# Performance work log

Hardware: AMD Instinct MI355X
Metric: run time of the kernel (lower is better)

The kernel has to match this reference:

```python
import jax, jax.numpy as jnp
import numpy as np

N_NODES = 90  # hard-coded per-graph node count in the original module
HIDDEN = 128


def setup_inputs() -> dict:
    key = jax.random.key(0)
    ks = jax.random.split(key, 12)
    B = 8192
    adj = jax.random.uniform(ks[0], (B, N_NODES, N_NODES), dtype=jnp.float32)
    s_in = 1.0 / np.sqrt(N_NODES)
    s_h = 1.0 / np.sqrt(HIDDEN)
    return {
        "adj": adj,
        "W_mlp0": jax.random.normal(ks[1], (N_NODES, HIDDEN), jnp.float32) * s_in,
        "b_mlp0": jax.random.normal(ks[2], (HIDDEN,), jnp.float32) * s_in,
        "W_mlp1": jax.random.normal(ks[3], (HIDDEN, HIDDEN), jnp.float32) * s_h,
        "b_mlp1": jax.random.normal(ks[4], (HIDDEN,), jnp.float32) * s_h,
        "W_mlp2": jax.random.normal(ks[5], (HIDDEN, HIDDEN), jnp.float32) * s_h,
        "b_mlp2": jax.random.normal(ks[6], (HIDDEN,), jnp.float32) * s_h,
        "W_res1": jax.random.normal(ks[7], (HIDDEN, HIDDEN), jnp.float32) * s_h,
        "b_res1": jax.random.normal(ks[8], (HIDDEN,), jnp.float32) * s_h,
        "W_res2": jax.random.normal(ks[9], (HIDDEN, HIDDEN), jnp.float32) * s_h,
        "b_res2": jax.random.normal(ks[10], (HIDDEN,), jnp.float32) * s_h,
    }


def reference(adj, W_mlp0, b_mlp0, W_mlp1, b_mlp1, W_mlp2, b_mlp2,
              W_res1, b_res1, W_res2, b_res2):
    B = adj.shape[0]
    # raw node features: identity per graph (torch.eye(90) concatenated)
    raw_x = jnp.broadcast_to(jnp.eye(N_NODES, dtype=adj.dtype), (B, N_NODES, N_NODES))

    def gconv(x, W, b):
        # block-diagonal Adj_block @ x == batched per-graph matmul, then linear
        return jnp.einsum('bij,bjk->bik', adj, x) @ W + b

    # encoding == 1 branch, layers = 3
    h0 = gconv(raw_x, W_mlp0, b_mlp0)                    # mlps[0](raw_x, A)
    r1 = h0 @ W_res1 + b_res1                            # res[1](h0)
    x = jax.nn.relu(gconv(h0, W_mlp1, b_mlp1)) + r1      # layer 1
    Y = jax.nn.relu(gconv(x, W_mlp2, b_mlp2) + (r1 @ W_res2 + b_res2))  # final

    # decoder: per-graph inner-product, concatenated along node axis
    Z = jnp.einsum('bik,bjk->bij', Y, Y)                 # [B, 90, 90]
    return Z.reshape(B * N_NODES, N_NODES)
```

## Files before the change

### kernel.cpp

```cpp
#include <hip/hip_runtime.h>
#include <hip/hip_bf16.h>


#define NN 90
#define HH 128
#define NT 256

typedef _Float16 half8 __attribute__((ext_vector_type(8)));
typedef _Float16 half4 __attribute__((ext_vector_type(4)));
typedef float floatx16 __attribute__((ext_vector_type(16)));

#define SR 136
#define SR8 17
#define ST 104
#define ST8 13
#define ST4 26

#define MFMA(a, b, c) __builtin_amdgcn_mfma_f32_32x32x16_f16((a), (b), (c), 0, 0, 0)

__global__ void prep_weights(const float* __restrict__ W0,
                             const float* __restrict__ Wr1,
                             const float* __restrict__ W1,
                             const float* __restrict__ W2,
                             const float* __restrict__ Wr2,
                             _Float16* __restrict__ ws)
{
    const int idx = blockIdx.x * blockDim.x + threadIdx.x;
    if (idx >= 77824) return;
    if (idx < 12288) {
        const int n = idx / 96, k = idx - n * 96;
        ws[idx] = (k < NN) ? (_Float16)W0[k * HH + n] : (_Float16)0.f;
    } else {
        const int j = idx - 12288;
        const int m = j >> 14;
        const int r = j & 16383;
        const int n = r >> 7, k = r & 127;
        const float* src = (m == 0) ? Wr1 : (m == 1) ? W1 : (m == 2) ? W2 : Wr2;
        ws[idx] = (_Float16)src[k * HH + n];
    }
}

__global__ __launch_bounds__(NT) void graphcnn_mfma(
    const float* __restrict__ adj,
    const _Float16* __restrict__ wts,
    const float* __restrict__ b0, const float* __restrict__ b1,
    const float* __restrict__ b2, const float* __restrict__ br1,
    const float* __restrict__ br2,
    float* __restrict__ out)
{
    __shared__ __align__(16) unsigned char smem[98816];
    _Float16* adjH = (_Float16*)smem;
    _Float16* bufA = (_Float16*)(smem + 19968);
    _Float16* bufT = (_Float16*)(smem + 46080);
    _Float16* r1R  = (_Float16*)(smem + 72704);

    const int t    = threadIdx.x;
    const int wv   = t >> 6;
    const int lane = t & 63;
    const int p    = lane & 31;
    const int h    = lane >> 5;
    const int n    = wv * 32 + p;

    const _Float16* W0T  = wts;
    const _Float16* Wr1T = wts + 12288;
    const _Float16* W1T  = Wr1T + 16384;
    const _Float16* W2T  = W1T + 16384;
    const _Float16* Wr2T = W2T + 16384;

    for (int i = t; i < (96 * ST) / 2; i += NT) ((unsigned int*)adjH)[i] = 0u;
    __syncthreads();
    const float* Ag = adj + (size_t)blockIdx.x * (NN * NN);
    for (int i = t; i < NN * NN; i += NT) {
        const int r = i / NN, c = i - r * NN;
        adjH[r * ST + c] = (_Float16)Ag[i];
    }
    __syncthreads();

    auto writeR = [&](_Float16* buf, int mt, int col, const floatx16& A) {
        #pragma unroll
        for (int r = 0; r < 16; r++) {
            const int node = mt * 32 + (r & 3) + 8 * (r >> 2) + 4 * h;
            buf[node * SR + col] = (_Float16)A[r];
        }
    };
    auto writeT = [&](_Float16* buf, int mt, int col, const floatx16& A) {
        #pragma unroll
        for (int rg = 0; rg < 4; rg++) {
            half4 v = { (_Float16)A[4*rg], (_Float16)A[4*rg+1],
                        (_Float16)A[4*rg+2], (_Float16)A[4*rg+3] };
            ((half4*)buf)[col * ST4 + mt * 8 + 2 * rg + h] = v;
        }
    };

    floatx16 acc0, acc1, acc2;

    {
        half8 bf[6];
        #pragma unroll
        for (int kt = 0; kt < 6; kt++) bf[kt] = ((const half8*)W0T)[n * 12 + kt * 2 + h];
        const float bias = b0[n];
        #pragma unroll
        for (int r = 0; r < 16; r++) { acc0[r] = bias; acc1[r] = bias; acc2[r] = bias; }
        #pragma unroll
        for (int kt = 0; kt < 6; kt++) {
            half8 a0 = ((const half8*)adjH)[(0 * 32 + p) * ST8 + kt * 2 + h];
            half8 a1 = ((const half8*)adjH)[(1 * 32 + p) * ST8 + kt * 2 + h];
            half8 a2 = ((const half8*)adjH)[(2 * 32 + p) * ST8 + kt * 2 + h];
            acc0 = MFMA(a0, bf[kt], acc0);
            acc1 = MFMA(a1, bf[kt], acc1);
            acc2 = MFMA(a2, bf[kt], acc2);
        }
        writeR(bufA, 0, n, acc0); writeR(bufA, 1, n, acc1); writeR(bufA, 2, n, acc2);
        writeT(bufT, 0, n, acc0); writeT(bufT, 1, n, acc1); writeT(bufT, 2, n, acc2);
    }
    __syncthreads();

    {
        half8 bf[8];
        #pragma unroll
        for (int kt = 0; kt < 8; kt++) bf[kt] = ((const half8*)Wr1T)[n * 16 + kt * 2 + h];
        const float bias = br1[n];
        #pragma unroll
        for (int r = 0; r < 16; r++) { acc0[r] = bias; acc1[r] = bias; acc2[r] = bias; }
        #pragma unroll
        for (int kt = 0; kt < 8; kt++) {
            half8 a0 = ((const half8*)bufA)[(0 * 32 + p) * SR8 + kt * 2 + h];
            half8 a1 = ((const half8*)bufA)[(1 * 32 + p) * SR8 + kt * 2 + h];
            half8 a2 = ((const half8*)bufA)[(2 * 32 + p) * SR8 + kt * 2 + h];
            acc0 = MFMA(a0, bf[kt], acc0);
            acc1 = MFMA(a1, bf[kt], acc1);
            acc2 = MFMA(a2, bf[kt], acc2);
        }
        writeR(r1R, 0, n, acc0); writeR(r1R, 1, n, acc1); writeR(r1R, 2, n, acc2);
    }
    __syncthreads();

    {
        #pragma unroll
        for (int r = 0; r < 16; r++) { acc0[r] = 0.f; acc1[r] = 0.f; acc2[r] = 0.f; }
        #pragma unroll
        for (int kt = 0; kt < 6; kt++) {
            half8 bfk = ((const half8*)bufT)[n * ST8 + kt * 2 + h];
            half8 a0 = ((const half8*)adjH)[(0 * 32 + p) * ST8 + kt * 2 + h];
            half8 a1 = ((const half8*)adjH)[(1 * 32 + p) * ST8 + kt * 2 + h];
            half8 a2 = ((const half8*)adjH)[(2 * 32 + p) * ST8 + kt * 2 + h];
            acc0 = MFMA(a0, bfk, acc0);
            acc1 = MFMA(a1, bfk, acc1);
            acc2 = MFMA(a2, bfk, acc2);
        }
        writeR(bufA, 0, n, acc0); writeR(bufA, 1, n, acc1); writeR(bufA, 2, n, acc2);
    }
    __syncthreads();

    {
        half8 bf[8];
        #pragma unroll
        for (int kt = 0; kt < 8; kt++) bf[kt] = ((const half8*)W1T)[n * 16 + kt * 2 + h];
        const float bias = b1[n];
        #pragma unroll
        for (int r = 0; r < 16; r++) { acc0[r] = bias; acc1[r] = bias; acc2[r] = bias; }
        #pragma unroll
        for (int kt = 0; kt < 8; kt++) {
            half8 a0 = ((const half8*)bufA)[(0 * 32 + p) * SR8 + kt * 2 + h];
            half8 a1 = ((const half8*)bufA)[(1 * 32 + p) * SR8 + kt * 2 + h];
            half8 a2 = ((const half8*)bufA)[(2 * 32 + p) * SR8 + kt * 2 + h];
            acc0 = MFMA(a0, bf[kt], acc0);
            acc1 = MFMA(a1, bf[kt], acc1);
            acc2 = MFMA(a2, bf[kt], acc2);
        }
        #pragma unroll
        for (int mt = 0; mt < 3; mt++) {
            floatx16& A = (mt == 0) ? acc0 : (mt == 1) ? acc1 : acc2;
            floatx16 xv;
            #pragma unroll
            for (int r = 0; r < 16; r++) {
                const int node = mt * 32 + (r & 3) + 8 * (r >> 2) + 4 * h;
                xv[r] = fmaxf(A[r], 0.f) + (float)r1R[node * SR + n];
            }
            writeT(bufT, mt, n, xv);
        }
    }
    __syncthreads();

    {
        #pragma unroll
        for (int r = 0; r < 16; r++) { acc0[r] = 0.f; acc1[r] = 0.f; acc2[r] = 0.f; }
        #pragma unroll
        for (int kt = 0; kt < 6; kt++) {
            half8 bfk = ((const half8*)bufT)[n * ST8 + kt * 2 + h];
            half8 a0 = ((const half8*)adjH)[(0 * 32 + p) * ST8 + kt * 2 + h];
            half8 a1 = ((const half8*)adjH)[(1 * 32 + p) * ST8 + kt * 2 + h];
            half8 a2 = ((const half8*)adjH)[(2 * 32 + p) * ST8 + kt * 2 + h];
            acc0 = MFMA(a0, bfk, acc0);
            acc1 = MFMA(a1, bfk, acc1);
            acc2 = MFMA(a2, bfk, acc2);
        }
        writeR(bufA, 0, n, acc0); writeR(bufA, 1, n, acc1); writeR(bufA, 2, n, acc2);
    }
    __syncthreads();

    {
        half8 bf[8];
        #pragma unroll
        for (int kt = 0; kt < 8; kt++) bf[kt] = ((const half8*)W2T)[n * 16 + kt * 2 + h];
        const float bias = b2[n] + br2[n];
        #pragma unroll
        for (int r = 0; r < 16; r++) { acc0[r] = bias; acc1[r] = bias; acc2[r] = bias; }
        #pragma unroll
        for (int kt = 0; kt < 8; kt++) {
            half8 a0 = ((const half8*)bufA)[(0 * 32 + p) * SR8 + kt * 2 + h];
            half8 a1 = ((const half8*)bufA)[(1 * 32 + p) * SR8 + kt * 2 + h];
            half8 a2 = ((const half8*)bufA)[(2 * 32 + p) * SR8 + kt * 2 + h];
            acc0 = MFMA(a0, bf[kt], acc0);
            acc1 = MFMA(a1, bf[kt], acc1);
            acc2 = MFMA(a2, bf[kt], acc2);
        }
        half8 bg[8];
        #pragma unroll
        for (int kt = 0; kt < 8; kt++) bg[kt] = ((const half8*)Wr2T)[n * 16 + kt * 2 + h];
        #pragma unroll
        for (int kt = 0; kt < 8; kt++) {
            half8 a0 = ((const half8*)r1R)[(0 * 32 + p) * SR8 + kt * 2 + h];
            half8 a1 = ((const half8*)r1R)[(1 * 32 + p) * SR8 + kt * 2 + h];
            half8 a2 = ((const half8*)r1R)[(2 * 32 + p) * SR8 + kt * 2 + h];
            acc0 = MFMA(a0, bg[kt], acc0);
            acc1 = MFMA(a1, bg[kt], acc1);
            acc2 = MFMA(a2, bg[kt], acc2);
        }
        _Float16* YR = bufT;
        #pragma unroll
        for (int mt = 0; mt < 3; mt++) {
            floatx16& A = (mt == 0) ? acc0 : (mt == 1) ? acc1 : acc2;
            #pragma unroll
            for (int r = 0; r < 16; r++) {
                const int node = mt * 32 + (r & 3) + 8 * (r >> 2) + 4 * h;
                YR[node * SR + n] = (_Float16)fmaxf(A[r], 0.f);
            }
        }
    }
    __syncthreads();

    {
        const _Float16* YR = bufT;
        float* outb = out + (size_t)blockIdx.x * (NN * NN);
        auto ztile = [&](int mt, int nt) {
            floatx16 acc;
            #pragma unroll
            for (int r = 0; r < 16; r++) acc[r] = 0.f;
            #pragma unroll
            for (int kt = 0; kt < 8; kt++) {
                half8 av = ((const half8*)YR)[(mt * 32 + p) * SR8 + kt * 2 + h];
                half8 bv = ((const half8*)YR)[(nt * 32 + p) * SR8 + kt * 2 + h];
                acc = MFMA(av, bv, acc);
            }
            const int col = nt * 32 + p;
            if (col < NN) {
                #pragma unroll
                for (int r = 0; r < 16; r++) {
                    const int row = mt * 32 + (r & 3) + 8 * (r >> 2) + 4 * h;
                    if (row < NN) outb[row * NN + col] = acc[r];
                }
            }
        };
        if      (wv == 0) { ztile(0, 0); ztile(0, 1); ztile(0, 2); }
        else if (wv == 1) { ztile(1, 0); ztile(1, 1); }
        else if (wv == 2) { ztile(1, 2); ztile(2, 0); }
        else              { ztile(2, 1); ztile(2, 2); }
    }
}

extern "C" void kernel_launch(void* const* d_in, const int* in_sizes, int n_in,
                              void* d_out, int out_size, void* d_ws, size_t ws_size,
                              hipStream_t stream) {
    const float* adj = (const float*)d_in[0];
    const float* W0  = (const float*)d_in[1];
    const float* b0  = (const float*)d_in[2];
    const float* W1  = (const float*)d_in[3];
    const float* b1  = (const float*)d_in[4];
    const float* W2  = (const float*)d_in[5];
    const float* b2  = (const float*)d_in[6];
    const float* Wr1 = (const float*)d_in[7];
    const float* br1 = (const float*)d_in[8];
    const float* Wr2 = (const float*)d_in[9];
    const float* br2 = (const float*)d_in[10];
    float* out = (float*)d_out;
    _Float16* wts = (_Float16*)d_ws;

    prep_weights<<<76, 1024, 0, stream>>>(W0, Wr1, W1, W2, Wr2, wts);

    const int B = in_sizes[0] / (NN * NN);
    graphcnn_mfma<<<B, NT, 0, stream>>>(adj, wts, b0, b1, b2, br1, br2, out);
}
```

Baseline: 824.3 us.

## Fold residual weights, keep features in registers, cut LDS for two blocks per CU

Precomputes Wr1·Wr2 and the combined final bias in the prep kernel, so the r1@Wr2 path becomes h0@Wc and the r1 buffer no longer needs to live in shared memory. The transposed operand for the adjacency matmuls is built in registers through cross-half-wave shuffles instead of a transposed LDS buffer. The adjacency load is vectorised as float2. Shared memory drops from about 99KB to 72KB and launch bounds ask for 2 blocks per CU to raise occupancy. The trade-off is more register pressure from keeping r1 accumulators and fragments live, plus fp16 rounding of the folded weight product.

New measurement: 749.0 us. 9.1% less time.

```diff
diff --git a/kernel.cpp b/kernel.cpp
--- a/kernel.cpp
+++ b/kernel.cpp
@@ -1,5 +1,4 @@
 #include <hip/hip_runtime.h>
-#include <hip/hip_bf16.h>
 
 
 #define NN 90
@@ -7,14 +6,15 @@
 #define NT 256
 
 typedef _Float16 half8 __attribute__((ext_vector_type(8)));
-typedef _Float16 half4 __attribute__((ext_vector_type(4)));
+typedef _Float16 half2v __attribute__((ext_vector_type(2)));
 typedef float floatx16 __attribute__((ext_vector_type(16)));
-
+typedef unsigned int uint4v __attribute__((ext_vector_type(4)));
+
+#define AST 104
+#define AST8 13
+#define ASTU 52
 #define SR 136
 #define SR8 17
-#define ST 104
-#define ST8 13
-#define ST4 26
 
 #define MFMA(a, b, c) __builtin_amdgcn_mfma_f32_32x32x16_f16((a), (b), (c), 0, 0, 0)
 
@@ -23,36 +23,48 @@
                              const float* __restrict__ W1,
                              const float* __restrict__ W2,
                              const float* __restrict__ Wr2,
+                             const float* __restrict__ b2,
+                             const float* __restrict__ br1,
+                             const float* __restrict__ br2,
                              _Float16* __restrict__ ws)
 {
     const int idx = blockIdx.x * blockDim.x + threadIdx.x;
-    if (idx >= 77824) return;
     if (idx < 12288) {
-        const int n = idx / 96, k = idx - n * 96;
-        ws[idx] = (k < NN) ? (_Float16)W0[k * HH + n] : (_Float16)0.f;
-    } else {
+        const int nn = idx / 96, k = idx - nn * 96;
+        if (k != 90)
+            ws[idx] = (k < NN) ? (_Float16)W0[k * HH + nn] : (_Float16)0.f;
+    } else if (idx < 61440) {
         const int j = idx - 12288;
         const int m = j >> 14;
         const int r = j & 16383;
-        const int n = r >> 7, k = r & 127;
-        const float* src = (m == 0) ? Wr1 : (m == 1) ? W1 : (m == 2) ? W2 : Wr2;
-        ws[idx] = (_Float16)src[k * HH + n];
+        const int nn = r >> 7, k = r & 127;
+        const float* src = (m == 0) ? Wr1 : (m == 1) ? W1 : W2;
+        ws[idx] = (_Float16)src[k * HH + nn];
+    } else if (idx < 77824) {
+        const int j = idx - 61440;
+        const int nn = j >> 7, k = j & 127;
+        float s = 0.f;
+        for (int q = 0; q < HH; q++) s += Wr1[k * HH + q] * Wr2[q * HH + nn];
+        ws[idx] = (_Float16)s;
+    } else if (idx < 77952) {
+        const int nn = idx - 77824;
+        float s = b2[nn] + br2[nn];
+        for (int q = 0; q < HH; q++) s += br1[q] * Wr2[q * HH + nn];
+        ws[nn * 96 + 90] = (_Float16)s;
     }
 }
 
-__global__ __launch_bounds__(NT) void graphcnn_mfma(
+__global__ __launch_bounds__(NT, 2) void graphcnn_mfma(
     const float* __restrict__ adj,
     const _Float16* __restrict__ wts,
     const float* __restrict__ b0, const float* __restrict__ b1,
-    const float* __restrict__ b2, const float* __restrict__ br1,
-    const float* __restrict__ br2,
+    const float* __restrict__ br1,
     float* __restrict__ out)
 {
-    __shared__ __align__(16) unsigned char smem[98816];
+    __shared__ __align__(16) unsigned char smem[72192];
     _Float16* adjH = (_Float16*)smem;
-    _Float16* bufA = (_Float16*)(smem + 19968);
-    _Float16* bufT = (_Float16*)(smem + 46080);
-    _Float16* r1R  = (_Float16*)(smem + 72704);
+    _Float16* B1   = (_Float16*)(smem + 19968);
+    _Float16* B2   = (_Float16*)(smem + 46080);
 
     const int t    = threadIdx.x;
     const int wv   = t >> 6;
@@ -63,122 +75,151 @@
 
     const _Float16* W0T  = wts;
     const _Float16* Wr1T = wts + 12288;
-    const _Float16* W1T  = Wr1T + 16384;
-    const _Float16* W2T  = W1T + 16384;
-    const _Float16* Wr2T = W2T + 16384;
-
-    for (int i = t; i < (96 * ST) / 2; i += NT) ((unsigned int*)adjH)[i] = 0u;
-    __syncthreads();
-    const float* Ag = adj + (size_t)blockIdx.x * (NN * NN);
-    for (int i = t; i < NN * NN; i += NT) {
-        const int r = i / NN, c = i - r * NN;
-        adjH[r * ST + c] = (_Float16)Ag[i];
-    }
-    __syncthreads();
-
-    auto writeR = [&](_Float16* buf, int mt, int col, const floatx16& A) {
-        #pragma unroll
-        for (int r = 0; r < 16; r++) {
-            const int node = mt * 32 + (r & 3) + 8 * (r >> 2) + 4 * h;
-            buf[node * SR + col] = (_Float16)A[r];
+    const _Float16* W1T  = wts + 28672;
+    const _Float16* W2T  = wts + 45056;
+    const _Float16* WcT  = wts + 61440;
+
+    {
+        const float* Ag = adj + (size_t)blockIdx.x * (NN * NN);
+        unsigned* aH = (unsigned*)adjH;
+        #pragma unroll
+        for (int it = 0; it < 18; it++) {
+            const int i = t + it * NT;
+            const int r = i / 48, cc = i - r * 48;
+            unsigned val = 0u;
+            if (r < NN && cc < 45) {
+                const float2 v = *(const float2*)(Ag + r * NN + cc * 2);
+                const half2v hv = { (_Float16)v.x, (_Float16)v.y };
+                val = __builtin_bit_cast(unsigned, hv);
+            }
+            aH[r * ASTU + cc] = val;
+        }
+    }
+
+    auto writeR = [&](_Float16* buf, const floatx16& A0, const floatx16& A1,
+                      const floatx16& A2) {
+        #pragma unroll
+        for (int mt = 0; mt < 3; mt++) {
+            const floatx16& A = (mt == 0) ? A0 : (mt == 1) ? A1 : A2;
+            #pragma unroll
+            for (int r = 0; r < 16; r++) {
+                const int node = mt * 32 + (r & 3) + 8 * (r >> 2) + 4 * h;
+                buf[node * SR + n] = (_Float16)A[r];
+            }
         }
     };
-    auto writeT = [&](_Float16* buf, int mt, int col, const floatx16& A) {
-        #pragma unroll
-        for (int rg = 0; rg < 4; rg++) {
-            half4 v = { (_Float16)A[4*rg], (_Float16)A[4*rg+1],
-                        (_Float16)A[4*rg+2], (_Float16)A[4*rg+3] };
-            ((half4*)buf)[col * ST4 + mt * 8 + 2 * rg + h] = v;
+
+    uint4v frg[6];
+    auto buildFrags = [&](const floatx16& A0, const floatx16& A1, const floatx16& A2) {
+        #pragma unroll
+        for (int mt = 0; mt < 3; mt++) {
+            const floatx16& A = (mt == 0) ? A0 : (mt == 1) ? A1 : A2;
+            #pragma unroll
+            for (int s01 = 0; s01 < 2; s01++) {
+                const int s = 8 * s01;
+                const half2v x0 = { (_Float16)A[s + 0], (_Float16)A[s + 1] };
+                const half2v x1 = { (_Float16)A[s + 2], (_Float16)A[s + 3] };
+                const half2v y0 = { (_Float16)A[s + 4], (_Float16)A[s + 5] };
+                const half2v y1 = { (_Float16)A[s + 6], (_Float16)A[s + 7] };
+                const unsigned X0 = __builtin_bit_cast(unsigned, x0);
+                const unsigned X1 = __builtin_bit_cast(unsigned, x1);
+                const unsigned Y0 = __builtin_bit_cast(unsigned, y0);
+                const unsigned Y1 = __builtin_bit_cast(unsigned, y1);
+                const unsigned R0 = __shfl_xor(h ? X0 : Y0, 32, 64);
+                const unsigned R1 = __shfl_xor(h ? X1 : Y1, 32, 64);
+                uint4v f;
+                f[0] = h ? R0 : X0;
+                f[1] = h ? R1 : X1;
+                f[2] = h ? Y0 : R0;
+                f[3] = h ? Y1 : R1;
+                frg[mt * 2 + s01] = f;
+            }
         }
     };
 
+    __syncthreads();
+
     floatx16 acc0, acc1, acc2;
 
     {
-        half8 bf[6];
-        #pragma unroll
-        for (int kt = 0; kt < 6; kt++) bf[kt] = ((const half8*)W0T)[n * 12 + kt * 2 + h];
+        half8 bw[6];
+        #pragma unroll
+        for (int kt = 0; kt < 6; kt++) bw[kt] = ((const half8*)W0T)[n * 12 + kt * 2 + h];
         const float bias = b0[n];
         #pragma unroll
         for (int r = 0; r < 16; r++) { acc0[r] = bias; acc1[r] = bias; acc2[r] = bias; }
         #pragma unroll
         for (int kt = 0; kt < 6; kt++) {
-            half8 a0 = ((const half8*)adjH)[(0 * 32 + p) * ST8 + kt * 2 + h];
-            half8 a1 = ((const half8*)adjH)[(1 * 32 + p) * ST8 + kt * 2 + h];
-            half8 a2 = ((const half8*)adjH)[(2 * 32 + p) * ST8 + kt * 2 + h];
-            acc0 = MFMA(a0, bf[kt], acc0);
-            acc1 = MFMA(a1, bf[kt], acc1);
-            acc2 = MFMA(a2, bf[kt], acc2);
-        }
-        writeR(bufA, 0, n, acc0); writeR(bufA, 1, n, acc1); writeR(bufA, 2, n, acc2);
-        writeT(bufT, 0, n, acc0); writeT(bufT, 1, n, acc1); writeT(bufT, 2, n, acc2);
-    }
-    __syncthreads();
-
-    {
-        half8 bf[8];
-        #pragma unroll
-        for (int kt = 0; kt < 8; kt++) bf[kt] = ((const half8*)Wr1T)[n * 16 + kt * 2 + h];
-        const float bias = br1[n];
-        #pragma unroll
-        for (int r = 0; r < 16; r++) { acc0[r] = bias; acc1[r] = bias; acc2[r] = bias; }
-        #pragma unroll
-        for (int kt = 0; kt < 8; kt++) {
-            half8 a0 = ((const half8*)bufA)[(0 * 32 + p) * SR8 + kt * 2 + h];
-            half8 a1 = ((const half8*)bufA)[(1 * 32 + p) * SR8 + kt * 2 + h];
-            half8 a2 = ((const half8*)bufA)[(2 * 32 + p) * SR8 + kt * 2 + h];
-            acc0 = MFMA(a0, bf[kt], acc0);
-            acc1 = MFMA(a1, bf[kt], acc1);
-            acc2 = MFMA(a2, bf[kt], acc2);
-        }
-        writeR(r1R, 0, n, acc0); writeR(r1R, 1, n, acc1); writeR(r1R, 2, n, acc2);
-    }
-    __syncthreads();
+            const half8 a0 = ((const half8*)adjH)[(0 * 32 + p) * AST8 + kt * 2 + h];
+            const half8 a1 = ((const half8*)adjH)[(1 * 32 + p) * AST8 + kt * 2 + h];
+            const half8 a2 = ((const half8*)adjH)[(2 * 32 + p) * AST8 + kt * 2 + h];
+            acc0 = MFMA(a0, bw[kt], acc0);
+            acc1 = MFMA(a1, bw[kt], acc1);
+            acc2 = MFMA(a2, bw[kt], acc2);
+        }
+        writeR(B2, acc0, acc1, acc2);
+        buildFrags(acc0, acc1, acc2);
+    }
 
     {
         #pragma unroll
         for (int r = 0; r < 16; r++) { acc0[r] = 0.f; acc1[r] = 0.f; acc2[r] = 0.f; }
         #pragma unroll
         for (int kt = 0; kt < 6; kt++) {
-            half8 bfk = ((const half8*)bufT)[n * ST8 + kt * 2 + h];
-            half8 a0 = ((const half8*)adjH)[(0 * 32 + p) * ST8 + kt * 2 + h];
-            half8 a1 = ((const half8*)adjH)[(1 * 32 + p) * ST8 + kt * 2 + h];
-            half8 a2 = ((const half8*)adjH)[(2 * 32 + p) * ST8 + kt * 2 + h];
+            const half8 bfk = __builtin_bit_cast(half8, frg[kt]);
+            const half8 a0 = ((const half8*)adjH)[(0 * 32 + p) * AST8 + kt * 2 + h];
+            const half8 a1 = ((const half8*)adjH)[(1 * 32 + p) * AST8 + kt * 2 + h];
+            const half8 a2 = ((const half8*)adjH)[(2 * 32 + p) * AST8 + kt * 2 + h];
             acc0 = MFMA(a0, bfk, acc0);
             acc1 = MFMA(a1, bfk, acc1);
             acc2 = MFMA(a2, bfk, acc2);
         }
-        writeR(bufA, 0, n, acc0); writeR(bufA, 1, n, acc1); writeR(bufA, 2, n, acc2);
-    }
-    __syncthreads();
-
-    {
-        half8 bf[8];
-        #pragma unroll
-        for (int kt = 0; kt < 8; kt++) bf[kt] = ((const half8*)W1T)[n * 16 + kt * 2 + h];
+        writeR(B1, acc0, acc1, acc2);
+    }
+    __syncthreads();
+
+    floatx16 r1a, r1b, r1c;
+    {
+        half8 bw[8];
+        #pragma unroll
+        for (int kt = 0; kt < 8; kt++) bw[kt] = ((const half8*)Wr1T)[n * 16 + kt * 2 + h];
+        const float bias = br1[n];
+        #pragma unroll
+        for (int r = 0; r < 16; r++) { r1a[r] = bias; r1b[r] = bias; r1c[r] = bias; }
+        #pragma unroll
+        for (int kt = 0; kt < 8; kt++) {
+            const half8 a0 = ((const half8*)B2)[(0 * 32 + p) * SR8 + kt * 2 + h];
+            const half8 a1 = ((const half8*)B2)[(1 * 32 + p) * SR8 + kt * 2 + h];
+            const half8 a2 = ((const half8*)B2)[(2 * 32 + p) * SR8 + kt * 2 + h];
+            r1a = MFMA(a0, bw[kt], r1a);
+            r1b = MFMA(a1, bw[kt], r1b);
+            r1c = MFMA(a2, bw[kt], r1c);
+        }
+    }
+
+    {
+        half8 bw[8];
+        #pragma unroll
+        for (int kt = 0; kt < 8; kt++) bw[kt] = ((const half8*)W1T)[n * 16 + kt * 2 + h];
         const float bias = b1[n];
         #pragma unroll
         for (int r = 0; r < 16; r++) { acc0[r] = bias; acc1[r] = bias; acc2[r] = bias; }
         #pragma unroll
         for (int kt = 0; kt < 8; kt++) {
-            half8 a0 = ((const half8*)bufA)[(0 * 32 + p) * SR8 + kt * 2 + h];
-            half8 a1 = ((const half8*)bufA)[(1 * 32 + p) * SR8 + kt * 2 + h];
-            half8 a2 = ((const half8*)bufA)[(2 * 32 + p) * SR8 + kt * 2 + h];
-            acc0 = MFMA(a0, bf[kt], acc0);
-            acc1 = MFMA(a1, bf[kt], acc1);
-            acc2 = MFMA(a2, bf[kt], acc2);
-        }
-        #pragma unroll
-        for (int mt = 0; mt < 3; mt++) {
-            floatx16& A = (mt == 0) ? acc0 : (mt == 1) ? acc1 : acc2;
-            floatx16 xv;
-            #pragma unroll
-            for (int r = 0; r < 16; r++) {
-                const int node = mt * 32 + (r & 3) + 8 * (r >> 2) + 4 * h;
-                xv[r] = fmaxf(A[r], 0.f) + (float)r1R[node * SR + n];
-            }
-            writeT(bufT, mt, n, xv);
-        }
+            const half8 a0 = ((const half8*)B1)[(0 * 32 + p) * SR8 + kt * 2 + h];
+            const half8 a1 = ((const half8*)B1)[(1 * 32 + p) * SR8 + kt * 2 + h];
+            const half8 a2 = ((const half8*)B1)[(2 * 32 + p) * SR8 + kt * 2 + h];
+            acc0 = MFMA(a0, bw[kt], acc0);
+            acc1 = MFMA(a1, bw[kt], acc1);
+            acc2 = MFMA(a2, bw[kt], acc2);
+        }
+        #pragma unroll
+        for (int r = 0; r < 16; r++) {
+            acc0[r] = fmaxf(acc0[r], 0.f) + r1a[r];
+            acc1[r] = fmaxf(acc1[r], 0.f) + r1b[r];
+            acc2[r] = fmaxf(acc2[r], 0.f) + r1c[r];
+        }
+        buildFrags(acc0, acc1, acc2);
     }
     __syncthreads();
 
@@ -187,50 +228,53 @@
         for (int r = 0; r < 16; r++) { acc0[r] = 0.f; acc1[r] = 0.f; acc2[r] = 0.f; }
         #pragma unroll
         for (int kt = 0; kt < 6; kt++) {
-            half8 bfk = ((const half8*)bufT)[n * ST8 + kt * 2 + h];
-            half8 a0 = ((const half8*)adjH)[(0 * 32 + p) * ST8 + kt * 2 + h];
-            half8 a1 = ((const half8*)adjH)[(1 * 32 + p) * ST8 + kt * 2 + h];
-            half8 a2 = ((const half8*)adjH)[(2 * 32 + p) * ST8 + kt * 2 + h];
+            const half8 bfk = __builtin_bit_cast(half8, frg[kt]);
+            const half8 a0 = ((const half8*)adjH)[(0 * 32 + p) * AST8 + kt * 2 + h];
+            const half8 a1 = ((const half8*)adjH)[(1 * 32 + p) * AST8 + kt * 2 + h];
+            const half8 a2 = ((const half8*)adjH)[(2 * 32 + p) * AST8 + kt * 2 + h];
             acc0 = MFMA(a0, bfk, acc0);
             acc1 = MFMA(a1, bfk, acc1);
             acc2 = MFMA(a2, bfk, acc2);
         }
-        writeR(bufA, 0, n, acc0); writeR(bufA, 1, n, acc1); writeR(bufA, 2, n, acc2);
-    }
-    __syncthreads();
-
-    {
-        half8 bf[8];
-        #pragma unroll
-        for (int kt = 0; kt < 8; kt++) bf[kt] = ((const half8*)W2T)[n * 16 + kt * 2 + h];
-        const float bias = b2[n] + br2[n];
+        writeR(B1, acc0, acc1, acc2);
+    }
+    __syncthreads();
+
+    {
+        half8 bw[8], bg[8];
+        #pragma unroll
+        for (int kt = 0; kt < 8; kt++) {
+            bw[kt] = ((const half8*)W2T)[n * 16 + kt * 2 + h];
+            bg[kt] = ((const half8*)WcT)[n * 16 + kt * 2 + h];
+        }
+        const float bias = (float)W0T[n * 96 + 90];
         #pragma unroll
         for (int r = 0; r < 16; r++) { acc0[r] = bias; acc1[r] = bias; acc2[r] = bias; }
         #pragma unroll
         for (int kt = 0; kt < 8; kt++) {
-            half8 a0 = ((const half8*)bufA)[(0 * 32 + p) * SR8 + kt * 2 + h];
-            half8 a1 = ((const half8*)bufA)[(1 * 32 + p) * SR8 + kt * 2 + h];
-            half8 a2 = ((const half8*)bufA)[(2 * 32 + p) * SR8 + kt * 2 + h];
-            acc0 = MFMA(a0, bf[kt], acc0);
-            acc1 = MFMA(a1, bf[kt], acc1);
-            acc2 = MFMA(a2, bf[kt], acc2);
-        }
-        half8 bg[8];
-        #pragma unroll
-        for (int kt = 0; kt < 8; kt++) bg[kt] = ((const half8*)Wr2T)[n * 16 + kt * 2 + h];
-        #pragma unroll
-        for (int kt = 0; kt < 8; kt++) {
-            half8 a0 = ((const half8*)r1R)[(0 * 32 + p) * SR8 + kt * 2 + h];
-            half8 a1 = ((const half8*)r1R)[(1 * 32 + p) * SR8 + kt * 2 + h];
-            half8 a2 = ((const half8*)r1R)[(2 * 32 + p) * SR8 + kt * 2 + h];
+            const half8 a0 = ((const half8*)B1)[(0 * 32 + p) * SR8 + kt * 2 + h];
+            const half8 a1 = ((const half8*)B1)[(1 * 32 + p) * SR8 + kt * 2 + h];
+            const half8 a2 = ((const half8*)B1)[(2 * 32 + p) * SR8 + kt * 2 + h];
+            acc0 = MFMA(a0, bw[kt], acc0);
+            acc1 = MFMA(a1, bw[kt], acc1);
+            acc2 = MFMA(a2, bw[kt], acc2);
+        }
+        #pragma unroll
+        for (int kt = 0; kt < 8; kt++) {
+            const half8 a0 = ((const half8*)B2)[(0 * 32 + p) * SR8 + kt * 2 + h];
+            const half8 a1 = ((const half8*)B2)[(1 * 32 + p) * SR8 + kt * 2 + h];
+            const half8 a2 = ((const half8*)B2)[(2 * 32 + p) * SR8 + kt * 2 + h];
             acc0 = MFMA(a0, bg[kt], acc0);
             acc1 = MFMA(a1, bg[kt], acc1);
             acc2 = MFMA(a2, bg[kt], acc2);
         }
-        _Float16* YR = bufT;
+    }
+    __syncthreads();
+    {
+        _Float16* YR = B2;
         #pragma unroll
         for (int mt = 0; mt < 3; mt++) {
-            floatx16& A = (mt == 0) ? acc0 : (mt == 1) ? acc1 : acc2;
+            const floatx16& A = (mt == 0) ? acc0 : (mt == 1) ? acc1 : acc2;
             #pragma unroll
             for (int r = 0; r < 16; r++) {
                 const int node = mt * 32 + (r & 3) + 8 * (r >> 2) + 4 * h;
@@ -241,7 +285,7 @@
     __syncthreads();
 
     {
-        const _Float16* YR = bufT;
+        const _Float16* YR = B2;
         float* outb = out + (size_t)blockIdx.x * (NN * NN);
         auto ztile = [&](int mt, int nt) {
             floatx16 acc;
@@ -249,8 +293,8 @@
             for (int r = 0; r < 16; r++) acc[r] = 0.f;
             #pragma unroll
             for (int kt = 0; kt < 8; kt++) {
-                half8 av = ((const half8*)YR)[(mt * 32 + p) * SR8 + kt * 2 + h];
-                half8 bv = ((const half8*)YR)[(nt * 32 + p) * SR8 + kt * 2 + h];
+                const half8 av = ((const half8*)YR)[(mt * 32 + p) * SR8 + kt * 2 + h];
+                const half8 bv = ((const half8*)YR)[(nt * 32 + p) * SR8 + kt * 2 + h];
                 acc = MFMA(av, bv, acc);
             }
             const int col = nt * 32 + p;
@@ -286,8 +330,8 @@
     float* out = (float*)d_out;
     _Float16* wts = (_Float16*)d_ws;
 
-    prep_weights<<<76, 1024, 0, stream>>>(W0, Wr1, W1, W2, Wr2, wts);
+    prep_weights<<<77, 1024, 0, stream>>>(W0, Wr1, W1, W2, Wr2, b2, br1, br2, wts);
 
     const int B = in_sizes[0] / (NN * NN);
-    graphcnn_mfma<<<B, NT, 0, stream>>>(adj, wts, b0, b1, b2, br1, br2, out);
+    graphcnn_mfma<<<B, NT, 0, stream>>>(adj, wts, b0, b1, br1, out);
 }
```
